# Performance work log

Hardware: AMD Instinct MI355X
Metric: run time of the kernel (lower is better)

The kernel has to match this reference:

```python
import jax, jax.numpy as jnp
import numpy as np

# Constructor constants (from init_kwargs)
B, F, K, D = 4096, 2048, 64, 8
VOL_TEMP = 0.5   # SoftVolume temperature -> softplus beta = 1/VOL_TEMP
INT_TEMP = 0.1   # GumbelIntersection temperature
EPS = 1e-23      # box_embeddings soft-volume clamp


def setup_inputs() -> dict:
    key = jax.random.key(0)
    ks = jax.random.split(key, 9)
    def lin(k, shp, fan_in):
        return (jax.random.normal(k, shp, jnp.float32) / np.sqrt(fan_in)).astype(jnp.float32)
    return {
        "features": jax.random.normal(ks[0], (B, F), jnp.float32),
        # stacked per-concept projectors: Linear(F -> 2D) for each of K concepts
        "Wp": lin(ks[1], (K, F, 2 * D), F),
        "bp": lin(ks[2], (K, 2 * D), F),
        # stacked per-concept prob predictors: Linear(2D -> 1)
        "Wprob": lin(ks[3], (K, 2 * D), 2 * D),
        "bprob": lin(ks[4], (K,), 2 * D),
        # classifier heads
        "Wbox": lin(ks[5], (K * 2 * D, 1), K * 2 * D),
        "bbox": lin(ks[6], (1,), K * 2 * D),
        "Wrel": lin(ks[7], (K * K, 1), K * K),
        "brel": lin(ks[8], (1,), K * K),
    }


def _log_soft_volume(z, Z):
    # box_embeddings SoftVolume: sum_d log(max(softplus(Z - z, beta=1/vol_temp), eps))
    beta = 1.0 / VOL_TEMP
    side = jax.nn.softplus(beta * (Z - z)) / beta
    return jnp.sum(jnp.log(jnp.maximum(side, EPS)), axis=-1)


def reference(features, Wp, bp, Wprob, bprob, Wbox, bbox, Wrel, brel):
    b = features.shape[0]
    # all K projectors as one batched GEMM: [B,F] x [K,F,2D] -> [B,K,2D]
    theta = jnp.einsum('bf,kfd->bkd', features, Wp) + bp
    theta = theta.reshape(b, K, 2, D)
    # MinDeltaBoxTensor: z = theta[...,0,:], Z = z + softplus(theta[...,1,:])
    z = theta[:, :, 0, :]                       # [B,K,D]
    Z = z + jax.nn.softplus(theta[:, :, 1, :])  # [B,K,D]

    coords = jnp.concatenate([z, Z], axis=-1)   # [B,K,2D]
    logits = jnp.einsum('bkd,kd->bk', coords, Wprob) + bprob
    concept_probs = jax.nn.sigmoid(logits)      # [B,K]

    # Pairwise Gumbel intersection over all (i,j) concept pairs (vectorized k^2 loop)
    t = INT_TEMP
    zi, zj = z[:, :, None, :], z[:, None, :, :]   # [B,K,1,D] vs [B,1,K,D]
    Zi, Zj = Z[:, :, None, :], Z[:, None, :, :]
    z_int = t * jnp.logaddexp(zi / t, zj / t)
    z_int = jnp.maximum(z_int, jnp.maximum(zi, zj))
    Z_int = -t * jnp.logaddexp(-Zi / t, -Zj / t)
    Z_int = jnp.minimum(Z_int, jnp.minimum(Zi, Zj))

    lv_int = _log_soft_volume(z_int, Z_int)       # [B,K,K]
    lv_box = _log_soft_volume(z, Z)               # [B,K]
    # P(i|j) = vol(i ^ j) / vol(j)
    cond = jnp.clip(jnp.exp(lv_int - lv_box[:, None, :]), 1e-6, 1.0 - 1e-6)  # [B,K,K]

    # scale each box's coords by its concept prob, flatten as [z_i, Z_i] per concept
    p = concept_probs[:, :, None]
    flat_boxes = jnp.concatenate([z * p, Z * p], axis=-1).reshape(b, K * 2 * D)
    flat_rel = cond.reshape(b, K * K)

    final_logit = flat_boxes @ Wbox + bbox + flat_rel @ Wrel + brel  # [B,1]
    task_probs = jax.nn.sigmoid(final_logit)
    return task_probs, concept_probs, cond
```

## Files before the change

### kernel.cpp

```cpp
#include <hip/hip_runtime.h>
#include <cstdint>
#include <cstddef>


typedef __bf16 bf16_t;
typedef __bf16 bf16x4 __attribute__((ext_vector_type(4)));
typedef __bf16 bf16x8 __attribute__((ext_vector_type(8)));
typedef float floatx4 __attribute__((ext_vector_type(4)));

#define LOG2E 1.4426950408889634f
#define LN2 0.6931471805599453f
#define K1C 14.426950408889634f
#define K3C 2.8853900817779268f

__device__ __forceinline__ float ex2(float x) { return __builtin_exp2f(x); }
__device__ __forceinline__ float lg2(float x) { return __builtin_log2f(x); }

__device__ __forceinline__ void gload16(const bf16_t* g, bf16_t* l) {
  __builtin_amdgcn_global_load_lds(
      (const __attribute__((address_space(1))) void*)g,
      (__attribute__((address_space(3))) void*)l, 16, 0, 0);
}

__global__ __launch_bounds__(256, 2) void prep_ab(
    const float* __restrict__ A, bf16_t* __restrict__ Ah,
    bf16_t* __restrict__ Al, const float* __restrict__ Wp,
    bf16_t* __restrict__ Bt) {
  __shared__ float tile[128][17];
  const int bid = blockIdx.x;
  const int t = threadIdx.x;
  if (bid < 4096) {
    const size_t i = ((size_t)bid * 256 + t) * 8;
    const float4 v0 = *reinterpret_cast<const float4*>(A + i);
    const float4 v1 = *reinterpret_cast<const float4*>(A + i + 4);
    const float x[8] = {v0.x, v0.y, v0.z, v0.w, v1.x, v1.y, v1.z, v1.w};
    bf16x8 h, l;
#pragma unroll
    for (int u = 0; u < 8; ++u) {
      const __bf16 hv = (__bf16)x[u];
      h[u] = hv;
      l[u] = (__bf16)(x[u] - (float)hv);
    }
    *reinterpret_cast<bf16x8*>(Ah + i) = h;
    *reinterpret_cast<bf16x8*>(Al + i) = l;
    return;
  }
  const int pb = bid - 4096;
  const int kc = pb >> 4;
  const int f0 = (pb & 15) * 128;
  {
    const int fl = t >> 1, dh = (t & 1) * 8;
    const float* g = Wp + ((size_t)kc * 2048 + f0 + fl) * 16 + dh;
    float4 v0 = *reinterpret_cast<const float4*>(g);
    float4 v1 = *reinterpret_cast<const float4*>(g + 4);
    tile[fl][dh + 0] = v0.x; tile[fl][dh + 1] = v0.y;
    tile[fl][dh + 2] = v0.z; tile[fl][dh + 3] = v0.w;
    tile[fl][dh + 4] = v1.x; tile[fl][dh + 5] = v1.y;
    tile[fl][dh + 6] = v1.z; tile[fl][dh + 7] = v1.w;
  }
  __syncthreads();
  {
    const int d = t >> 4, fi = (t & 15) * 8;
    float x[8];
#pragma unroll
    for (int u = 0; u < 8; ++u) x[u] = tile[fi + u][d];
    bf16x8 hv, lv;
#pragma unroll
    for (int u = 0; u < 8; ++u) {
      __bf16 h = (__bf16)x[u];
      hv[u] = h;
      lv[u] = (__bf16)(x[u] - (float)h);
    }
    const size_t row = (size_t)(kc * 16 + d) * 4096;
    *reinterpret_cast<bf16x8*>(Bt + row + f0 + fi) = hv;
    *reinterpret_cast<bf16x8*>(Bt + row + 2048 + f0 + fi) = lv;
  }
}

__global__ __launch_bounds__(256, 1) void gemm_theta(
    const bf16_t* __restrict__ Ahg, const bf16_t* __restrict__ Alg,
    const bf16_t* __restrict__ Bt, const float* __restrict__ bias,
    float* __restrict__ C) {
  __shared__ bf16_t lds[2][4][128 * 32];
  const int t = threadIdx.x;
  const int m0 = blockIdx.x * 128, n0 = blockIdx.y * 128;
  const int wave = t >> 6, lane = t & 63, quad = lane >> 4, l16 = lane & 15;
  const int wm = (wave >> 1) * 64, wn = (wave & 1) * 64;
  floatx4 acc[4][4] = {};

  const int srow = t >> 2;
  const int skey = (srow >> 1) & 3;
  const int c8 = (((t & 3) ^ skey)) * 8;
  const bf16_t* gAh0 = Ahg + (size_t)(m0 + srow) * 2048 + c8;
  const bf16_t* gAh1 = Ahg + (size_t)(m0 + 64 + srow) * 2048 + c8;
  const bf16_t* gAl0 = Alg + (size_t)(m0 + srow) * 2048 + c8;
  const bf16_t* gAl1 = Alg + (size_t)(m0 + 64 + srow) * 2048 + c8;
  const bf16_t* gBh0 = Bt + (size_t)(n0 + srow) * 4096 + c8;
  const bf16_t* gBh1 = Bt + (size_t)(n0 + 64 + srow) * 4096 + c8;

  auto stage = [&](int bf, int kk) {
    const int ko = kk * 32;
    gload16(gAh0 + ko, &lds[bf][0][t * 8]);
    gload16(gAh1 + ko, &lds[bf][0][(256 + t) * 8]);
    gload16(gAl0 + ko, &lds[bf][1][t * 8]);
    gload16(gAl1 + ko, &lds[bf][1][(256 + t) * 8]);
    gload16(gBh0 + ko, &lds[bf][2][t * 8]);
    gload16(gBh1 + ko, &lds[bf][2][(256 + t) * 8]);
    gload16(gBh0 + 2048 + ko, &lds[bf][3][t * 8]);
    gload16(gBh1 + 2048 + ko, &lds[bf][3][(256 + t) * 8]);
  };

  stage(0, 0);
  __syncthreads();

  const int fkey = (l16 >> 1) & 3;
  const int qa = (quad ^ fkey) * 8;

  int buf = 0;
  for (int kk = 0; kk < 64; ++kk) {
    if (kk < 63) stage(buf ^ 1, kk + 1);
    bf16x8 ah[4], al[4], bh[4], bl[4];
#pragma unroll
    for (int r = 0; r < 4; ++r) {
      const int off = (wm + r * 16 + l16) * 32 + qa;
      ah[r] = *reinterpret_cast<const bf16x8*>(&lds[buf][0][off]);
      al[r] = *reinterpret_cast<const bf16x8*>(&lds[buf][1][off]);
    }
#pragma unroll
    for (int c = 0; c < 4; ++c) {
      const int off = (wn + c * 16 + l16) * 32 + qa;
      bh[c] = *reinterpret_cast<const bf16x8*>(&lds[buf][2][off]);
      bl[c] = *reinterpret_cast<const bf16x8*>(&lds[buf][3][off]);
    }
#pragma unroll
    for (int r = 0; r < 4; ++r)
#pragma unroll
      for (int c = 0; c < 4; ++c) {
        acc[r][c] = __builtin_amdgcn_mfma_f32_16x16x32_bf16(ah[r], bh[c],
                                                            acc[r][c], 0, 0, 0);
        acc[r][c] = __builtin_amdgcn_mfma_f32_16x16x32_bf16(al[r], bh[c],
                                                            acc[r][c], 0, 0, 0);
        acc[r][c] = __builtin_amdgcn_mfma_f32_16x16x32_bf16(ah[r], bl[c],
                                                            acc[r][c], 0, 0, 0);
      }
    __syncthreads();
    buf ^= 1;
  }

#pragma unroll
  for (int r = 0; r < 4; ++r) {
    const int row0 = m0 + wm + r * 16 + quad * 4;
#pragma unroll
    for (int c = 0; c < 4; ++c) {
      const int col = n0 + wn + c * 16 + l16;
      const float bb = bias[col];
#pragma unroll
      for (int i = 0; i < 4; ++i)
        C[(size_t)(row0 + i) * 1024 + col] = acc[r][c][i] + bb;
    }
  }
}

__global__ __launch_bounds__(256, 4) void fused_pair(
    const float* __restrict__ Th, const float* __restrict__ Wprob,
    const float* __restrict__ bprob, const float* __restrict__ Wbox,
    const float* __restrict__ bbox, const float* __restrict__ Wrel,
    const float* __restrict__ brel, float* __restrict__ out) {
  __shared__ float sboxes[64][17];
  __shared__ float spinv[64];
  __shared__ float spc[64];
  __shared__ float swrel[4096];
  __shared__ float swbox[1024];
  __shared__ float sprod[2080];
  __shared__ float sred[4];

  const int b = blockIdx.x;
  const int t = threadIdx.x;
  const float* th = Th + (size_t)b * 1024;
  float* out_task = out;
  float* out_conc = out + 4096;
  float* out_cond = out + 266240;

  if (t < 64) {
    const int k = t;
    const float* thk = th + k * 16;
    float4 a0 = reinterpret_cast<const float4*>(thk)[0];
    float4 a1 = reinterpret_cast<const float4*>(thk)[1];
    float4 a2 = reinterpret_cast<const float4*>(thk)[2];
    float4 a3 = reinterpret_cast<const float4*>(thk)[3];
    float z[8] = {a0.x, a0.y, a0.z, a0.w, a1.x, a1.y, a1.z, a1.w};
    float w1[8] = {a2.x, a2.y, a2.z, a2.w, a3.x, a3.y, a3.z, a3.w};
    float dp = 1.0f;
    float logit = bprob[k];
#pragma unroll
    for (int d = 0; d < 8; ++d) {
      const float spv = LN2 * lg2(1.0f + ex2(w1[d] * LOG2E));
      const float Zd = z[d] + spv;
      const float denl = lg2(1.0f + ex2((Zd - z[d]) * K3C));
      dp *= denl;
      logit += z[d] * Wprob[k * 16 + d] + Zd * Wprob[k * 16 + 8 + d];
      sboxes[k][d] = z[d];
      sboxes[k][8 + d] = Zd;
    }
    spinv[k] = 1.0f / dp;
    const float pk = 1.0f / (1.0f + ex2(-logit * LOG2E));
    spc[k] = pk;
    out_conc[(size_t)b * 64 + k] = pk;
  }
#pragma unroll
  for (int q = 0; q < 4; ++q)
    reinterpret_cast<float4*>(swrel)[q * 256 + t] =
        reinterpret_cast<const float4*>(Wrel)[q * 256 + t];
  reinterpret_cast<float4*>(swbox)[t] = reinterpret_cast<const float4*>(Wbox)[t];
  __syncthreads();

#pragma unroll
  for (int q = 0; q < 9; ++q) {
    const int p = t + 256 * q;
    if (p < 2080) {
      int j = (int)((sqrtf((float)(8 * p + 1)) - 1.0f) * 0.5f);
      if ((j + 1) * (j + 2) / 2 <= p) ++j;
      if (j * (j + 1) / 2 > p) --j;
      const int i = p - j * (j + 1) / 2;
      float prodn = 1.0f;
#pragma unroll
      for (int d = 0; d < 8; ++d) {
        const float zi = sboxes[i][d], Zi = sboxes[i][8 + d];
        const float zjd = sboxes[j][d], Zjd = sboxes[j][8 + d];
        const float u = ex2(-fabsf(zi - zjd) * K1C);
        const float uZ = ex2(-fabsf(Zi - Zjd) * K1C);
        const float lsum = lg2(fmaf(u, uZ, 1.0f + u + uZ));
        const float gap = fminf(Zi, Zjd) - fmaxf(zi, zjd);
        const float E = ex2(fmaf(gap, K3C, -0.2f * lsum));
        prodn *= lg2(1.0f + E);
      }
      sprod[p] = prodn;
    }
  }
  __syncthreads();

  const int wv = t >> 6, lane = t & 63;
  const float pinvj = spinv[lane];
  float rsum = 0.0f;
#pragma unroll 4
  for (int ii = 0; ii < 16; ++ii) {
    const int i = wv * 16 + ii;
    const int lo = min(i, lane), hi = max(i, lane);
    const float prodn = sprod[hi * (hi + 1) / 2 + lo];
    float cond = prodn * pinvj;
    cond = fminf(fmaxf(cond, 1e-6f), 1.0f - 1e-6f);
    out_cond[(size_t)b * 4096 + i * 64 + lane] = cond;
    rsum = fmaf(cond, swrel[i * 64 + lane], rsum);
  }

  float bsum = 0.0f;
#pragma unroll
  for (int q = 0; q < 4; ++q) {
    const int idx = t + 256 * q;
    const int k = idx >> 4, c = idx & 15;
    bsum = fmaf(sboxes[k][c] * spc[k], swbox[idx], bsum);
  }
  float total = rsum + bsum;
#pragma unroll
  for (int off = 32; off > 0; off >>= 1) total += __shfl_down(total, off, 64);
  if (lane == 0) sred[wv] = total;
  __syncthreads();
  if (t == 0) {
    const float s = sred[0] + sred[1] + sred[2] + sred[3] + bbox[0] + brel[0];
    out_task[b] = 1.0f / (1.0f + ex2(-s * LOG2E));
  }
}

extern "C" void kernel_launch(void* const* d_in, const int* in_sizes, int n_in,
                              void* d_out, int out_size, void* d_ws, size_t ws_size,
                              hipStream_t stream) {
  const float* feat = (const float*)d_in[0];
  const float* Wp = (const float*)d_in[1];
  const float* bp = (const float*)d_in[2];
  const float* Wprob = (const float*)d_in[3];
  const float* bprob = (const float*)d_in[4];
  const float* Wbox = (const float*)d_in[5];
  const float* bbox = (const float*)d_in[6];
  const float* Wrel = (const float*)d_in[7];
  const float* brel = (const float*)d_in[8];
  float* out = (float*)d_out;

  char* ws = (char*)d_ws;
  bf16_t* Bt = (bf16_t*)ws;
  float* Th = (float*)(ws + (size_t)(8 << 20));
  bf16_t* Ah = (bf16_t*)(ws + (size_t)(24 << 20));
  bf16_t* Al = (bf16_t*)(ws + (size_t)(40 << 20));

  prep_ab<<<5120, 256, 0, stream>>>(feat, Ah, Al, Wp, Bt);
  gemm_theta<<<dim3(32, 8), 256, 0, stream>>>(Ah, Al, Bt, bp, Th);
  fused_pair<<<4096, 256, 0, stream>>>(Th, Wprob, bprob, Wbox, bbox, Wrel, brel, out);
}
```

Baseline: 277.7 us.

## Halve GEMM M-tile for more blocks and replace transcendental calls with polynomials

Measured after the change: 291.5 us. 5.0% more time.

```diff
diff --git a/kernel.cpp b/kernel.cpp
--- a/kernel.cpp
+++ b/kernel.cpp
@@ -15,6 +15,32 @@
 
 __device__ __forceinline__ float ex2(float x) { return __builtin_exp2f(x); }
 __device__ __forceinline__ float lg2(float x) { return __builtin_log2f(x); }
+
+__device__ __forceinline__ float fex2(float x) {
+  x = fmaxf(x, -126.0f);
+  const float fl = __builtin_floorf(x);
+  const float f = x - fl;
+  float p = 1.5403530393381609e-4f;
+  p = fmaf(p, f, 1.3333558146428443e-3f);
+  p = fmaf(p, f, 9.618129107628477e-3f);
+  p = fmaf(p, f, 5.550410866482158e-2f);
+  p = fmaf(p, f, 2.402265069591007e-1f);
+  p = fmaf(p, f, 6.931471805599453e-1f);
+  p = fmaf(p, f, 1.0f);
+  return __builtin_ldexpf(p, (int)fl);
+}
+
+__device__ __forceinline__ float h01(float x) {
+  const float w = fmaf(x, 0.6666666666666666f, -0.3333333333333333f);
+  float p = 0.20609929155556620f;
+  p = fmaf(p, w, -0.24044917348149390f);
+  p = fmaf(p, w, 0.28853900817779270f);
+  p = fmaf(p, w, -0.36067376022224086f);
+  p = fmaf(p, w, 0.48089834696298780f);
+  p = fmaf(p, w, -0.72134752044448170f);
+  p = fmaf(p, w, 1.44269504088896340f);
+  return fmaf(p, w, 0.5849625007211562f);
+}
 
 __device__ __forceinline__ void gload16(const bf16_t* g, bf16_t* l) {
   __builtin_amdgcn_global_load_lds(
@@ -77,37 +103,36 @@
   }
 }
 
-__global__ __launch_bounds__(256, 1) void gemm_theta(
+__global__ __launch_bounds__(256, 2) void gemm_theta(
     const bf16_t* __restrict__ Ahg, const bf16_t* __restrict__ Alg,
     const bf16_t* __restrict__ Bt, const float* __restrict__ bias,
     float* __restrict__ C) {
-  __shared__ bf16_t lds[2][4][128 * 32];
+  __shared__ bf16_t Ah2[2][64 * 32];
+  __shared__ bf16_t Al2[2][64 * 32];
+  __shared__ bf16_t Bh2[2][128 * 32];
+  __shared__ bf16_t Bl2[2][128 * 32];
   const int t = threadIdx.x;
-  const int m0 = blockIdx.x * 128, n0 = blockIdx.y * 128;
+  const int m0 = blockIdx.x * 64, n0 = blockIdx.y * 128;
   const int wave = t >> 6, lane = t & 63, quad = lane >> 4, l16 = lane & 15;
-  const int wm = (wave >> 1) * 64, wn = (wave & 1) * 64;
-  floatx4 acc[4][4] = {};
+  const int wm = (wave >> 1) * 32, wn = (wave & 1) * 64;
+  floatx4 acc[2][4] = {};
 
   const int srow = t >> 2;
   const int skey = (srow >> 1) & 3;
   const int c8 = (((t & 3) ^ skey)) * 8;
   const bf16_t* gAh0 = Ahg + (size_t)(m0 + srow) * 2048 + c8;
-  const bf16_t* gAh1 = Ahg + (size_t)(m0 + 64 + srow) * 2048 + c8;
   const bf16_t* gAl0 = Alg + (size_t)(m0 + srow) * 2048 + c8;
-  const bf16_t* gAl1 = Alg + (size_t)(m0 + 64 + srow) * 2048 + c8;
   const bf16_t* gBh0 = Bt + (size_t)(n0 + srow) * 4096 + c8;
   const bf16_t* gBh1 = Bt + (size_t)(n0 + 64 + srow) * 4096 + c8;
 
   auto stage = [&](int bf, int kk) {
     const int ko = kk * 32;
-    gload16(gAh0 + ko, &lds[bf][0][t * 8]);
-    gload16(gAh1 + ko, &lds[bf][0][(256 + t) * 8]);
-    gload16(gAl0 + ko, &lds[bf][1][t * 8]);
-    gload16(gAl1 + ko, &lds[bf][1][(256 + t) * 8]);
-    gload16(gBh0 + ko, &lds[bf][2][t * 8]);
-    gload16(gBh1 + ko, &lds[bf][2][(256 + t) * 8]);
-    gload16(gBh0 + 2048 + ko, &lds[bf][3][t * 8]);
-    gload16(gBh1 + 2048 + ko, &lds[bf][3][(256 + t) * 8]);
+    gload16(gAh0 + ko, &Ah2[bf][t * 8]);
+    gload16(gAl0 + ko, &Al2[bf][t * 8]);
+    gload16(gBh0 + ko, &Bh2[bf][t * 8]);
+    gload16(gBh1 + ko, &Bh2[bf][(256 + t) * 8]);
+    gload16(gBh0 + 2048 + ko, &Bl2[bf][t * 8]);
+    gload16(gBh1 + 2048 + ko, &Bl2[bf][(256 + t) * 8]);
   };
 
   stage(0, 0);
@@ -119,21 +144,21 @@
   int buf = 0;
   for (int kk = 0; kk < 64; ++kk) {
     if (kk < 63) stage(buf ^ 1, kk + 1);
-    bf16x8 ah[4], al[4], bh[4], bl[4];
-#pragma unroll
-    for (int r = 0; r < 4; ++r) {
+    bf16x8 ah[2], al[2], bh[4], bl[4];
+#pragma unroll
+    for (int r = 0; r < 2; ++r) {
       const int off = (wm + r * 16 + l16) * 32 + qa;
-      ah[r] = *reinterpret_cast<const bf16x8*>(&lds[buf][0][off]);
-      al[r] = *reinterpret_cast<const bf16x8*>(&lds[buf][1][off]);
+      ah[r] = *reinterpret_cast<const bf16x8*>(&Ah2[buf][off]);
+      al[r] = *reinterpret_cast<const bf16x8*>(&Al2[buf][off]);
     }
 #pragma unroll
     for (int c = 0; c < 4; ++c) {
       const int off = (wn + c * 16 + l16) * 32 + qa;
-      bh[c] = *reinterpret_cast<const bf16x8*>(&lds[buf][2][off]);
-      bl[c] = *reinterpret_cast<const bf16x8*>(&lds[buf][3][off]);
-    }
-#pragma unroll
-    for (int r = 0; r < 4; ++r)
+      bh[c] = *reinterpret_cast<const bf16x8*>(&Bh2[buf][off]);
+      bl[c] = *reinterpret_cast<const bf16x8*>(&Bl2[buf][off]);
+    }
+#pragma unroll
+    for (int r = 0; r < 2; ++r)
 #pragma unroll
       for (int c = 0; c < 4; ++c) {
         acc[r][c] = __builtin_amdgcn_mfma_f32_16x16x32_bf16(ah[r], bh[c],
@@ -148,7 +173,7 @@
   }
 
 #pragma unroll
-  for (int r = 0; r < 4; ++r) {
+  for (int r = 0; r < 2; ++r) {
     const int row0 = m0 + wm + r * 16 + quad * 4;
 #pragma unroll
     for (int c = 0; c < 4; ++c) {
@@ -227,9 +252,9 @@
       for (int d = 0; d < 8; ++d) {
         const float zi = sboxes[i][d], Zi = sboxes[i][8 + d];
         const float zjd = sboxes[j][d], Zjd = sboxes[j][8 + d];
-        const float u = ex2(-fabsf(zi - zjd) * K1C);
-        const float uZ = ex2(-fabsf(Zi - Zjd) * K1C);
-        const float lsum = lg2(fmaf(u, uZ, 1.0f + u + uZ));
+        const float u = fex2(-fabsf(zi - zjd) * K1C);
+        const float uZ = fex2(-fabsf(Zi - Zjd) * K1C);
+        const float lsum = h01(u) + h01(uZ);
         const float gap = fminf(Zi, Zjd) - fmaxf(zi, zjd);
         const float E = ex2(fmaf(gap, K3C, -0.2f * lsum));
         prodn *= lg2(1.0f + E);
@@ -292,6 +317,6 @@
   bf16_t* Al = (bf16_t*)(ws + (size_t)(40 << 20));
 
   prep_ab<<<5120, 256, 0, stream>>>(feat, Ah, Al, Wp, Bt);
-  gemm_theta<<<dim3(32, 8), 256, 0, stream>>>(Ah, Al, Bt, bp, Th);
+  gemm_theta<<<dim3(64, 8), 256, 0, stream>>>(Ah, Al, Bt, bp, Th);
   fused_pair<<<4096, 256, 0, stream>>>(Th, Wprob, bprob, Wbox, bbox, Wrel, brel, out);
 }
```
